# Optimization experiments

Measured on AMD Instinct MI355X. Metric: run time of the kernel, lower is better.

The kernel has to match this reference:

```python
import jax, jax.numpy as jnp
import numpy as np

B, HW, D = 16, 3600, 512
LC, NL = 768, 20
KC, VC, H = 512, 512, 8
EPS = 1e-5


def instance_norm(x):
    # x: [B, N, C]; InstanceNorm1d normalizes over the length dim N per (sample, channel),
    # biased variance, no affine (torch default).
    mu = jnp.mean(x, axis=1, keepdims=True)
    var = jnp.mean((x - mu) ** 2, axis=1, keepdims=True)
    return (x - mu) / jnp.sqrt(var + EPS)


def setup_inputs() -> dict:
    key = jax.random.key(0)
    ks = jax.random.split(key, 16)
    x = jax.random.normal(ks[0], (B, HW, D), dtype=jnp.float32)
    l = jax.random.normal(ks[1], (B, LC, NL), dtype=jnp.float32)
    # 0/1 padding mask; guarantee at least the first token is valid
    lengths = jax.random.randint(ks[2], (B, 1), 5, NL + 1)
    l_mask = (jnp.arange(NL)[None, :] < lengths).astype(jnp.float32)[:, :, None]  # [B,NL,1]
    s = 0.02
    params = dict(
        Wvis=jax.random.normal(ks[3], (D, D)) * s, bvis=jnp.zeros((D,)),
        Wq=jax.random.normal(ks[4], (KC, D)) * s, bq=jnp.zeros((KC,)),
        Wk=jax.random.normal(ks[5], (KC, LC)) * s, bk=jnp.zeros((KC,)),
        Wval=jax.random.normal(ks[6], (VC, LC)) * s, bval=jnp.zeros((VC,)),
        Ww=jax.random.normal(ks[7], (VC, VC)) * s, bw=jnp.zeros((VC,)),
        Wmm=jax.random.normal(ks[8], (VC, VC)) * s, bmm=jnp.zeros((VC,)),
    )
    return {"x": x, "l": l, "l_mask": l_mask, **params}


def reference(x, l, l_mask, Wvis, bvis, Wq, bq, Wk, bk, Wval, bval, Ww, bw, Wmm, bmm):
    b, hw, d = x.shape
    mask = l_mask[..., 0][:, None, :]  # [B,1,NL]
    # vis branch: Conv1d(dim,dim,1) + GELU (exact) + Dropout(0)
    vis = jax.nn.gelu(x @ Wvis.T + bvis, approximate=False)  # [B,HW,D]
    # query: Conv1d(v_in,KC,1) then InstanceNorm1d over HW
    q = instance_norm(x @ Wq.T + bq)  # [B,HW,KC]
    # key/value: Conv1d over language channels, then mask
    k = (jnp.einsum('kc,bcn->bkn', Wk, l) + bk[None, :, None]) * mask    # [B,KC,NL]
    v = (jnp.einsum('vc,bcn->bvn', Wval, l) + bval[None, :, None]) * mask  # [B,VC,NL]
    qh = q.reshape(b, hw, H, KC // H).transpose(0, 2, 1, 3)   # [B,H,HW,KC/H]
    kh = k.reshape(b, H, KC // H, NL)                         # [B,H,KC/H,NL]
    vh = v.reshape(b, H, VC // H, NL)                         # [B,H,VC/H,NL]
    sim = jnp.einsum('bhqd,bhdn->bhqn', qh, kh) * (KC ** -0.5)
    sim = sim + (10000.0 * mask[:, :, None, :] - 10000.0)     # additive mask bias
    attn = jax.nn.softmax(sim, axis=-1)
    out = jnp.einsum('bhqn,bhdn->bhqd', attn, vh)             # [B,H,HW,VC/H]
    out = out.transpose(0, 2, 1, 3).reshape(b, hw, VC)
    lang = instance_norm(out @ Ww.T + bw)                     # W: Conv1d + IN over HW
    mm = jax.nn.gelu((vis * lang) @ Wmm.T + bmm, approximate=False)
    return mm  # [B,HW,VC]
```

## Files before the change

### kernel.cpp

```cpp
#include <hip/hip_runtime.h>


#define B_   16
#define HW_  3600
#define D_   512
#define LC_  768
#define NL_  20

typedef __attribute__((ext_vector_type(8))) __bf16 bf16x8;
typedef __attribute__((ext_vector_type(4))) float f32x4;
typedef __attribute__((ext_vector_type(4))) float float4v;
typedef __attribute__((ext_vector_type(8))) unsigned short ushort8v;
typedef __attribute__((ext_vector_type(4))) unsigned short ushort4v;
typedef __attribute__((ext_vector_type(2))) unsigned int uint2v;

static __device__ __forceinline__ float bf2f(unsigned short u){
  unsigned int x = ((unsigned int)u) << 16; float f;
  __builtin_memcpy(&f, &x, 4); return f;
}
static __device__ __forceinline__ unsigned short f2bf(float f){
  __bf16 h = (__bf16)f;
  unsigned short u; __builtin_memcpy(&u, &h, 2); return u;
}
static __device__ __forceinline__ unsigned int pack2bf(float lo, float hi){
  return (unsigned int)f2bf(lo) | ((unsigned int)f2bf(hi) << 16);
}
static __device__ __forceinline__ float gelu_f(float x){
  float z  = x * 0.7071067811865476f;
  float az = fabsf(z);
  float t = 1.0f / fmaf(0.3275911f, az, 1.0f);
  float p = fmaf(1.061405429f, t, -1.453152027f);
  p = fmaf(p, t, 1.421413741f);
  p = fmaf(p, t, -0.284496736f);
  p = fmaf(p, t, 0.254829592f);
  p = p * t;
  float er = 1.0f - p * __expf(-az * az);
  er = copysignf(er, z);
  return 0.5f * x * (1.0f + er);
}

__global__ void k_cvt_all(const float* __restrict__ x,
                          const float* __restrict__ Wvis, const float* __restrict__ Wq,
                          const float* __restrict__ Ww,   const float* __restrict__ Wmm,
                          unsigned short* __restrict__ xb, unsigned short* __restrict__ wcat,
                          unsigned short* __restrict__ wwb, unsigned short* __restrict__ wmmb){
  const int NX4 = (B_ * HW_ * D_) / 4;
  const int TOT = NX4 + 4 * 65536;
  int i = blockIdx.x * 256 + threadIdx.x;
  int stride = gridDim.x * 256;
  for (; i < TOT; i += stride){
    const float4v* s; ushort4v* dp;
    if (i < NX4){
      s  = (const float4v*)x + i;
      dp = (ushort4v*)xb + i;
    } else {
      int k = i - NX4;
      int seg = k >> 16, o = k & 0xFFFF;
      if      (seg == 0){ s = (const float4v*)Wvis + o; dp = (ushort4v*)wcat + o; }
      else if (seg == 1){ s = (const float4v*)Wq   + o; dp = (ushort4v*)wcat + 65536 + o; }
      else if (seg == 2){ s = (const float4v*)Ww   + o; dp = (ushort4v*)wwb + o; }
      else              { s = (const float4v*)Wmm  + o; dp = (ushort4v*)wmmb + o; }
    }
    float4v v = *s;
    ushort4v u;
    u.x = f2bf(v.x); u.y = f2bf(v.y); u.z = f2bf(v.z); u.w = f2bf(v.w);
    *dp = u;
  }
}

__global__ void k_kv(const float* __restrict__ l, const float* __restrict__ l_mask,
                     const float* __restrict__ Wk, const float* __restrict__ bk,
                     const float* __restrict__ Wval, const float* __restrict__ bval,
                     float* __restrict__ k_s, float* __restrict__ v_s){
  const int b = blockIdx.y;
  const int part = blockIdx.x;
  const bool isK = part < 8;
  const int c0 = (part & 7) * 64;
  const float* W  = isK ? Wk : Wval;
  const float* bi = isK ? bk : bval;
  float* outp = isK ? k_s : v_s;

  __shared__ float l_sh[LC_ * NL_];
  for (int i = threadIdx.x; i < LC_ * NL_; i += 256)
    l_sh[i] = l[(size_t)b * LC_ * NL_ + i];
  __syncthreads();

  const int tid = threadIdx.x;
  const int cl = tid >> 2;
  const int q  = tid & 3;
  const int c  = c0 + cl;
  const float* wrow = W + (size_t)c * LC_;
  float acc[5] = {0.f,0.f,0.f,0.f,0.f};
  for (int i = 0; i < LC_; ++i){
    float wv = wrow[i];
    const float* lr = l_sh + i * NL_ + q * 5;
    acc[0] = fmaf(wv, lr[0], acc[0]);
    acc[1] = fmaf(wv, lr[1], acc[1]);
    acc[2] = fmaf(wv, lr[2], acc[2]);
    acc[3] = fmaf(wv, lr[3], acc[3]);
    acc[4] = fmaf(wv, lr[4], acc[4]);
  }
  const float bb = bi[c];
  #pragma unroll
  for (int n5 = 0; n5 < 5; ++n5){
    int n = q * 5 + n5;
    float m = l_mask[b * NL_ + n];
    float val = (acc[n5] + bb) * m;
    if (isK) val *= 0.04419417382415922f;
    outp[((size_t)b * 512 + c) * NL_ + n] = val;
  }
}

template<int MODE, int NT, bool STATS>
__global__ __launch_bounds__(256, 4) void k_gemm(
    const unsigned short* __restrict__ A,
    const unsigned short* __restrict__ Bm,
    const float* __restrict__ bias0, const float* __restrict__ bias1,
    unsigned short* __restrict__ o0, unsigned short* __restrict__ o1,
    float* __restrict__ of, float2* __restrict__ partial)
{
  __shared__ __align__(16) unsigned short smem[2][2][128 * 32];
  __shared__ float2 red[2][128];

  const int nwg = 29 * NT * B_;
  const int per = nwg >> 3;
  const int d = blockIdx.x;
  const int g = (d & 7) * per + (d >> 3);
  constexpr int NSH = (NT == 8) ? 3 : 2;
  const int nt = g & (NT - 1);
  const int rem = g >> NSH;
  const int mt = rem % 29;
  const int b  = rem / 29;

  const int m0 = mt * 128;
  const int n0 = nt * 128;
  const int tid = threadIdx.x;
  const int w = tid >> 6, lane = tid & 63;
  const int wr = w >> 1, wc = w & 1;
  const int lr_ = lane & 15, lg_ = lane >> 4;
  const int mvalid = HW_ - m0;
  const unsigned short* Ab = A + (size_t)b * HW_ * 512;

  f32x4 acc[4][4];
  #pragma unroll
  for (int i = 0; i < 4; ++i)
    #pragma unroll
    for (int j = 0; j < 4; ++j)
      acc[i][j] = (f32x4){0.f, 0.f, 0.f, 0.f};

  auto stage = [&](int kt, int buf){
    const int k0 = kt * 32;
    #pragma unroll
    for (int s = 0; s < 2; ++s){
      int chunk = s * 256 + tid;
      int row = chunk >> 2, part = chunk & 3;
      int psrc = part ^ ((row >> 1) & 3);
      int grow = row < mvalid ? row : (mvalid - 1);
      const unsigned short* gsrc = Ab + ((size_t)(m0 + grow) * 512 + k0 + psrc * 8);
      unsigned short* ldst = &smem[0][buf][(s * 256 + w * 64) * 8];
      __builtin_amdgcn_global_load_lds((const __attribute__((address_space(1))) void*)gsrc,
                                       (__attribute__((address_space(3))) void*)ldst, 16, 0, 0);
    }
    #pragma unroll
    for (int s = 0; s < 2; ++s){
      int chunk = s * 256 + tid;
      int row = chunk >> 2, part = chunk & 3;
      int psrc = part ^ ((row >> 1) & 3);
      const unsigned short* gsrc = Bm + ((size_t)(n0 + row) * 512 + k0 + psrc * 8);
      unsigned short* ldst = &smem[1][buf][(s * 256 + w * 64) * 8];
      __builtin_amdgcn_global_load_lds((const __attribute__((address_space(1))) void*)gsrc,
                                       (__attribute__((address_space(3))) void*)ldst, 16, 0, 0);
    }
  };

  auto compute = [&](int buf){
    const unsigned short* lA = &smem[0][buf][(wr * 64) * 32];
    const unsigned short* lB = &smem[1][buf][(wc * 64) * 32];
    const int kx = (lg_ ^ ((lr_ >> 1) & 3)) * 8;
    bf16x8 av[4], bv[4];
    #pragma unroll
    for (int i = 0; i < 4; ++i) av[i] = *(const bf16x8*)(lA + (i * 16 + lr_) * 32 + kx);
    #pragma unroll
    for (int j = 0; j < 4; ++j) bv[j] = *(const bf16x8*)(lB + (j * 16 + lr_) * 32 + kx);
    #pragma unroll
    for (int i = 0; i < 4; ++i)
      #pragma unroll
      for (int j = 0; j < 4; ++j)
        acc[i][j] = __builtin_amdgcn_mfma_f32_16x16x32_bf16(av[i], bv[j], acc[i][j], 0, 0, 0);
  };

  stage(0, 0);
  #pragma unroll
  for (int t = 0; t < 16; ++t){
    asm volatile("s_waitcnt lgkmcnt(0)" ::: "memory");
    __builtin_amdgcn_sched_barrier(0);
    asm volatile("s_waitcnt vmcnt(0)" ::: "memory");
    __builtin_amdgcn_s_barrier();
    __builtin_amdgcn_sched_barrier(0);
    if (t < 15) stage(t + 1, (t + 1) & 1);
    compute(t & 1);
  }

  const int colbase = n0 + wc * 64;
  float bsv[4];
  #pragma unroll
  for (int j = 0; j < 4; ++j){
    int col = colbase + j * 16 + lr_;
    if (MODE == 0) bsv[j] = (col < 512) ? bias0[col] : bias1[col - 512];
    else           bsv[j] = bias0[col];
  }
  const bool do_stats = STATS && (MODE != 0 || n0 >= 512);

  if (STATS && do_stats){
    float colsum[4] = {0.f,0.f,0.f,0.f}, colsq[4] = {0.f,0.f,0.f,0.f};
    #pragma unroll
    for (int i = 0; i < 4; ++i){
      int rowb = m0 + wr * 64 + i * 16 + lg_ * 4;
      #pragma unroll
      for (int rr = 0; rr < 4; ++rr){
        if (rowb + rr < HW_){
          #pragma unroll
          for (int j = 0; j < 4; ++j){
            float v = acc[i][j][rr] + bsv[j];
            colsum[j] += v;
            colsq[j]  = fmaf(v, v, colsq[j]);
          }
        }
      }
    }
    #pragma unroll
    for (int j = 0; j < 4; ++j){
      colsum[j] += __shfl_xor(colsum[j], 16);
      colsum[j] += __shfl_xor(colsum[j], 32);
      colsq[j]  += __shfl_xor(colsq[j], 16);
      colsq[j]  += __shfl_xor(colsq[j], 32);
    }
    if (lg_ == 0){
      #pragma unroll
      for (int j = 0; j < 4; ++j)
        red[wr][wc * 64 + j * 16 + lr_] = make_float2(colsum[j], colsq[j]);
    }
  }

  __syncthreads();

  if (STATS && do_stats && tid < 128){
    float2 r0 = red[0][tid], r1 = red[1][tid];
    int gcol = n0 + tid - (MODE == 0 ? 512 : 0);
    partial[((size_t)b * 29 + mt) * 512 + gcol] = make_float2(r0.x + r1.x, r0.y + r1.y);
  }

  unsigned short* stw = &smem[0][0][0] + w * 4096;

  if (MODE == 2){
    float* stgf = (float*)stw;
    #pragma unroll
    for (int half = 0; half < 2; ++half){
      #pragma unroll
      for (int i2 = 0; i2 < 2; ++i2){
        int i = half * 2 + i2;
        #pragma unroll
        for (int rr = 0; rr < 4; ++rr)
          #pragma unroll
          for (int j = 0; j < 4; ++j)
            stgf[(i2 * 16 + lg_ * 4 + rr) * 64 + j * 16 + lr_] = gelu_f(acc[i][j][rr] + bsv[j]);
      }
      #pragma unroll
      for (int pass = 0; pass < 8; ++pass){
        int chunk = pass * 64 + lane;
        int row = chunk >> 4, sub = chunk & 15;
        float4v vv = *(const float4v*)(stgf + row * 64 + sub * 4);
        int grow = m0 + wr * 64 + half * 32 + row;
        if (grow < HW_)
          *(float4v*)(of + ((size_t)b * HW_ + grow) * 512 + colbase + sub * 4) = vv;
      }
    }
  } else {
    #pragma unroll
    for (int i = 0; i < 4; ++i)
      #pragma unroll
      for (int rr = 0; rr < 4; ++rr)
        #pragma unroll
        for (int j = 0; j < 4; ++j){
          float v = acc[i][j][rr] + bsv[j];
          stw[(i * 16 + lg_ * 4 + rr) * 64 + j * 16 + lr_] = f2bf(v);
        }
    unsigned short* optr = (MODE == 1 || n0 < 512) ? o0 : o1;
    const int coloff = (MODE == 1 || n0 < 512) ? colbase : (colbase - 512);
    #pragma unroll
    for (int pass = 0; pass < 8; ++pass){
      int chunk = pass * 64 + lane;
      int row = chunk >> 3, sub = chunk & 7;
      ushort8v vv = *(const ushort8v*)(stw + row * 64 + sub * 8);
      int grow = m0 + wr * 64 + row;
      if (grow < HW_)
        *(ushort8v*)(optr + ((size_t)b * HW_ + grow) * 512 + coloff + sub * 8) = vv;
    }
  }
}

__global__ void k_stats_p2b(const float2* __restrict__ partial, float2* __restrict__ stats){
  const int b = blockIdx.x;
  const int c = threadIdx.x;
  float s = 0.f, q = 0.f;
  for (int mt = 0; mt < 29; ++mt){
    float2 p = partial[((size_t)b * 29 + mt) * 512 + c];
    s += p.x; q += p.y;
  }
  float mean = s * (1.0f / (float)HW_);
  float var  = q * (1.0f / (float)HW_) - mean * mean;
  stats[(size_t)b * 512 + c] = make_float2(mean, rsqrtf(var + 1e-5f));
}

__global__ void k_prep(const float2* __restrict__ partial, const float* __restrict__ k_s,
                       const float* __restrict__ v_s, const float* __restrict__ l_mask,
                       unsigned short* __restrict__ k2, unsigned short* __restrict__ v2,
                       float* __restrict__ e_s)
{
  const int b = blockIdx.x;
  const int tid = threadIdx.x;
  __shared__ float wred[4][NL_];
  __shared__ float2 stats_sh[512];

  #pragma unroll
  for (int half = 0; half < 2; ++half){
    int c = tid + half * 256;
    float s = 0.f, q = 0.f;
    for (int mt = 0; mt < 29; ++mt){
      float2 p = partial[((size_t)b * 29 + mt) * 512 + c];
      s += p.x; q += p.y;
    }
    float mean = s * (1.0f / (float)HW_);
    float var  = q * (1.0f / (float)HW_) - mean * mean;
    stats_sh[c] = make_float2(mean, rsqrtf(var + 1e-5f));
  }
  __syncthreads();

  float part[NL_];
  #pragma unroll
  for (int n = 0; n < NL_; ++n) part[n] = 0.f;
  #pragma unroll
  for (int half = 0; half < 2; ++half){
    int c = tid + half * 256;
    float2 st = stats_sh[c];
    float ms = st.x * st.y;
    const float* row = k_s + ((size_t)b * 512 + c) * NL_;
    #pragma unroll
    for (int n = 0; n < NL_; ++n) part[n] = fmaf(ms, row[n], part[n]);
  }
  #pragma unroll
  for (int n = 0; n < NL_; ++n){
    float v = part[n];
    v += __shfl_xor(v, 1);  v += __shfl_xor(v, 2);  v += __shfl_xor(v, 4);
    v += __shfl_xor(v, 8);  v += __shfl_xor(v, 16); v += __shfl_xor(v, 32);
    part[n] = v;
  }
  if ((tid & 63) == 0){
    #pragma unroll
    for (int n = 0; n < NL_; ++n) wred[tid >> 6][n] = part[n];
  }
  __syncthreads();
  if (tid < 32){
    float e;
    if (tid < NL_){
      float dsum = wred[0][tid] + wred[1][tid] + wred[2][tid] + wred[3][tid];
      e = -dsum - 10000.0f * (1.0f - l_mask[b * NL_ + tid]);
    } else {
      e = -1e30f;
    }
    e_s[b * 32 + tid] = e;
  }

  for (int i = tid; i < 16384; i += 256){
    int h = i >> 11, t = (i >> 10) & 1, s = (i >> 9) & 1;
    int l = (i >> 3) & 63, j = i & 7;
    int r = l & 15, g = l >> 4;
    int n = t * 16 + r;
    int c = h * 64 + s * 32 + g * 8 + j;
    unsigned short val = 0;
    if (n < NL_){
      float inv = stats_sh[c].y;
      val = f2bf(inv * k_s[((size_t)b * 512 + c) * NL_ + n]);
    }
    k2[(size_t)b * 16384 + i] = val;
  }
  for (int i = tid; i < 16384; i += 256){
    int h = i >> 11, ct = (i >> 9) & 3;
    int l = (i >> 3) & 63, j = i & 7;
    int r = l & 15, g = l >> 4;
    int n = g * 8 + j;
    int c = h * 64 + ct * 16 + r;
    unsigned short val = 0;
    if (n < NL_) val = f2bf(v_s[((size_t)b * 512 + c) * NL_ + n]);
    v2[(size_t)b * 16384 + i] = val;
  }
}

__global__ __launch_bounds__(256) void k_attn2(unsigned short* __restrict__ qraw,
    const unsigned short* __restrict__ k2, const unsigned short* __restrict__ v2,
    const float* __restrict__ e_s)
{
  const int b = blockIdx.y;
  const int w = threadIdx.x >> 6;
  const int tile = blockIdx.x * 4 + w;
  __shared__ __align__(16) unsigned short p_sh[4][16 * 32];
  __shared__ __align__(16) unsigned short o_sh[4][16 * 72];
  if (tile >= 225) return;
  const int lane = threadIdx.x & 63;
  const int r = lane & 15, g = lane >> 4;
  const int row0 = tile * 16;

  float4v e0 = *(const float4v*)(e_s + b * 32 + g * 4);
  float4v e1 = *(const float4v*)(e_s + b * 32 + 16 + g * 4);

  bf16x8 qf[8][2];
  const unsigned short* qbase = qraw + ((size_t)(b * HW_ + row0 + r) * 512) + g * 8;
  #pragma unroll
  for (int h = 0; h < 8; ++h)
    #pragma unroll
    for (int s = 0; s < 2; ++s)
      qf[h][s] = *(const bf16x8*)(qbase + h * 64 + s * 32);

  const unsigned short* kb = k2 + (size_t)b * 16384 + lane * 8;
  const unsigned short* vb = v2 + (size_t)b * 16384 + lane * 8;
  unsigned short* psh = &p_sh[w][0];
  unsigned short* osh = &o_sh[w][0];

  for (int h = 0; h < 8; ++h){
    bf16x8 kf00 = *(const bf16x8*)(kb + (h * 4 + 0) * 512);
    bf16x8 kf01 = *(const bf16x8*)(kb + (h * 4 + 1) * 512);
    bf16x8 kf10 = *(const bf16x8*)(kb + (h * 4 + 2) * 512);
    bf16x8 kf11 = *(const bf16x8*)(kb + (h * 4 + 3) * 512);
    f32x4 c0 = (f32x4){0.f,0.f,0.f,0.f};
    f32x4 c1 = (f32x4){0.f,0.f,0.f,0.f};
    c0 = __builtin_amdgcn_mfma_f32_16x16x32_bf16(kf00, qf[h][0], c0, 0, 0, 0);
    c0 = __builtin_amdgcn_mfma_f32_16x16x32_bf16(kf01, qf[h][1], c0, 0, 0, 0);
    c1 = __builtin_amdgcn_mfma_f32_16x16x32_bf16(kf10, qf[h][0], c1, 0, 0, 0);
    c1 = __builtin_amdgcn_mfma_f32_16x16x32_bf16(kf11, qf[h][1], c1, 0, 0, 0);

    float l0[4], l1[4];
    #pragma unroll
    for (int i = 0; i < 4; ++i){ l0[i] = c0[i] + e0[i]; l1[i] = c1[i] + e1[i]; }
    float m = fmaxf(fmaxf(fmaxf(l0[0], l0[1]), fmaxf(l0[2], l0[3])),
                    fmaxf(fmaxf(l1[0], l1[1]), fmaxf(l1[2], l1[3])));
    m = fmaxf(m, __shfl_xor(m, 16));
    m = fmaxf(m, __shfl_xor(m, 32));
    float p0[4], p1[4];
    #pragma unroll
    for (int i = 0; i < 4; ++i){ p0[i] = __expf(l0[i] - m); p1[i] = __expf(l1[i] - m); }

    uint2v pw0, pw1;
    pw0.x = pack2bf(p0[0], p0[1]); pw0.y = pack2bf(p0[2], p0[3]);
    pw1.x = pack2bf(p1[0], p1[1]); pw1.y = pack2bf(p1[2], p1[3]);
    float sum = bf2f((unsigned short)(pw0.x & 0xffff)) + bf2f((unsigned short)(pw0.x >> 16))
              + bf2f((unsigned short)(pw0.y & 0xffff)) + bf2f((unsigned short)(pw0.y >> 16))
              + bf2f((unsigned short)(pw1.x & 0xffff)) + bf2f((unsigned short)(pw1.x >> 16))
              + bf2f((unsigned short)(pw1.y & 0xffff)) + bf2f((unsigned short)(pw1.y >> 16));
    sum += __shfl_xor(sum, 16);
    sum += __shfl_xor(sum, 32);
    float inv = 1.0f / sum;

    *(uint2v*)(psh + r * 32 + 4 * g)      = pw0;
    *(uint2v*)(psh + r * 32 + 16 + 4 * g) = pw1;
    bf16x8 pfrag = *(const bf16x8*)(psh + r * 32 + g * 8);

    f32x4 dd[4];
    #pragma unroll
    for (int ct = 0; ct < 4; ++ct){
      bf16x8 vf = *(const bf16x8*)(vb + (h * 4 + ct) * 512);
      f32x4 z = (f32x4){0.f,0.f,0.f,0.f};
      dd[ct] = __builtin_amdgcn_mfma_f32_16x16x32_bf16(vf, pfrag, z, 0, 0, 0);
    }
    #pragma unroll
    for (int ct = 0; ct < 4; ++ct){
      uint2v ow;
      ow.x = pack2bf(dd[ct][0] * inv, dd[ct][1] * inv);
      ow.y = pack2bf(dd[ct][2] * inv, dd[ct][3] * inv);
      *(uint2v*)(osh + r * 72 + ct * 16 + 4 * g) = ow;
    }
    int frow = lane >> 2, fch = lane & 3;
    ushort8v t0 = *(const ushort8v*)(osh + frow * 72 + fch * 16);
    ushort8v t1 = *(const ushort8v*)(osh + frow * 72 + fch * 16 + 8);
    unsigned short* gdst = qraw + ((size_t)(b * HW_ + row0 + frow) * 512) + h * 64 + fch * 16;
    *(ushort8v*)(gdst)     = t0;
    *(ushort8v*)(gdst + 8) = t1;
  }
}

__global__ __launch_bounds__(256) void k_hmul(unsigned short* __restrict__ yw,
    const unsigned short* __restrict__ visb, const float2* __restrict__ stats)
{
  const int b = blockIdx.y, blk = blockIdx.x;
  const int w = threadIdx.x >> 6, lane = threadIdx.x & 63;
  const int c0 = lane * 8;
  float mean[8], inv[8];
  #pragma unroll
  for (int j = 0; j < 8; ++j){
    float2 st = stats[(size_t)b * 512 + c0 + j];
    mean[j] = st.x; inv[j] = st.y;
  }
  for (int it = 0; it < 30; ++it){
    int row = blk * 120 + it * 4 + w;
    size_t off = ((size_t)b * HW_ + row) * 512 + c0;
    ushort8v yv = *(const ushort8v*)(yw + off);
    ushort8v vv = *(const ushort8v*)(visb + off);
    ushort8v hv;
    #pragma unroll
    for (int j = 0; j < 8; ++j){
      float lang = (bf2f(yv[j]) - mean[j]) * inv[j];
      float visg = gelu_f(bf2f(vv[j]));
      hv[j] = f2bf(visg * lang);
    }
    *(ushort8v*)(yw + off) = hv;
  }
}

extern "C" void kernel_launch(void* const* d_in, const int* in_sizes, int n_in,
                              void* d_out, int out_size, void* d_ws, size_t ws_size,
                              hipStream_t stream)
{
  const float* x     = (const float*)d_in[0];
  const float* l     = (const float*)d_in[1];
  const float* lmask = (const float*)d_in[2];
  const float* Wvis  = (const float*)d_in[3];
  const float* bvis  = (const float*)d_in[4];
  const float* Wq    = (const float*)d_in[5];
  const float* bq    = (const float*)d_in[6];
  const float* Wk    = (const float*)d_in[7];
  const float* bk    = (const float*)d_in[8];
  const float* Wval  = (const float*)d_in[9];
  const float* bval  = (const float*)d_in[10];
  const float* Ww    = (const float*)d_in[11];
  const float* bw    = (const float*)d_in[12];
  const float* Wmm   = (const float*)d_in[13];
  const float* bmm   = (const float*)d_in[14];
  float* out = (float*)d_out;

  char* ws = (char*)d_ws;
  if (ws_size < 240517120ull) return;
  unsigned short* xb    = (unsigned short*)(ws + 0);
  unsigned short* visb  = (unsigned short*)(ws + 58982400);
  unsigned short* qraw  = (unsigned short*)(ws + 117964800);
  unsigned short* yw    = (unsigned short*)(ws + 176947200);
  unsigned short* wcat  = (unsigned short*)(ws + 235929600);
  unsigned short* wwb   = (unsigned short*)(ws + 236978176);
  unsigned short* wmmb  = (unsigned short*)(ws + 237502464);
  float*  k_s    = (float*)(ws + 238026752);
  float*  v_s    = (float*)(ws + 238682112);
  float2* stats_w= (float2*)(ws + 240451584);
  unsigned short* k2 = (unsigned short*)(ws + 0);
  unsigned short* v2 = (unsigned short*)(ws + 524288);
  float*          e_s = (float*)(ws + 1048576);
  float2* partial_q = (float2*)(ws + 176947200);
  float2* partial_w = (float2*)(ws + 1052672);

  k_cvt_all<<<2048, 256, 0, stream>>>(x, Wvis, Wq, Ww, Wmm, xb, wcat, wwb, wmmb);

  k_kv<<<dim3(16, B_), 256, 0, stream>>>(l, lmask, Wk, bk, Wval, bval, k_s, v_s);

  k_gemm<0, 8, true><<<29 * 8 * B_, 256, 0, stream>>>(xb, wcat, bvis, bq, visb, qraw, nullptr, partial_q);

  k_prep<<<B_, 256, 0, stream>>>(partial_q, k_s, v_s, lmask, k2, v2, e_s);

  k_attn2<<<dim3(57, B_), 256, 0, stream>>>(qraw, k2, v2, e_s);

  k_gemm<1, 4, true><<<29 * 4 * B_, 256, 0, stream>>>(qraw, wwb, bw, nullptr, yw, nullptr, nullptr, partial_w);

  k_stats_p2b<<<B_, 512, 0, stream>>>(partial_w, stats_w);

  k_hmul<<<dim3(30, B_), 256, 0, stream>>>(yw, visb, stats_w);

  k_gemm<2, 4, false><<<29 * 4 * B_, 256, 0, stream>>>(yw, wmmb, bmm, nullptr, nullptr, nullptr, out, nullptr);
}
```

Measured before the change: 357.6 us.

## Fuse fp32-to-bf16 conversion of x into first GEMM's A-tile staging

Drops the separate pass that converts x (about 118MB of fp32) to bf16. The first GEMM now loads fp32 A tiles into registers, converts them and writes them to LDS after compute, overlapping with the MFMA work. The per-block LDS reduction of column stats is replaced by writing per-warp-row partials directly to global memory, which doubles the partial buffer and the reads in the stats kernels. Launch bounds rise to 5 waves per SIMD. The trade-off is extra register pressure and fp32 global reads inside the GEMM, which now reads twice the bytes for the A operand.

```diff
diff --git a/kernel.cpp b/kernel.cpp
--- a/kernel.cpp
+++ b/kernel.cpp
@@ -39,28 +39,20 @@
   return 0.5f * x * (1.0f + er);
 }
 
-__global__ void k_cvt_all(const float* __restrict__ x,
-                          const float* __restrict__ Wvis, const float* __restrict__ Wq,
-                          const float* __restrict__ Ww,   const float* __restrict__ Wmm,
-                          unsigned short* __restrict__ xb, unsigned short* __restrict__ wcat,
-                          unsigned short* __restrict__ wwb, unsigned short* __restrict__ wmmb){
-  const int NX4 = (B_ * HW_ * D_) / 4;
-  const int TOT = NX4 + 4 * 65536;
+__global__ void k_cvt_w(const float* __restrict__ Wvis, const float* __restrict__ Wq,
+                        const float* __restrict__ Ww,   const float* __restrict__ Wmm,
+                        unsigned short* __restrict__ wcat,
+                        unsigned short* __restrict__ wwb, unsigned short* __restrict__ wmmb){
+  const int TOT = 4 * 65536;
   int i = blockIdx.x * 256 + threadIdx.x;
   int stride = gridDim.x * 256;
   for (; i < TOT; i += stride){
+    int seg = i >> 16, o = i & 0xFFFF;
     const float4v* s; ushort4v* dp;
-    if (i < NX4){
-      s  = (const float4v*)x + i;
-      dp = (ushort4v*)xb + i;
-    } else {
-      int k = i - NX4;
-      int seg = k >> 16, o = k & 0xFFFF;
-      if      (seg == 0){ s = (const float4v*)Wvis + o; dp = (ushort4v*)wcat + o; }
-      else if (seg == 1){ s = (const float4v*)Wq   + o; dp = (ushort4v*)wcat + 65536 + o; }
-      else if (seg == 2){ s = (const float4v*)Ww   + o; dp = (ushort4v*)wwb + o; }
-      else              { s = (const float4v*)Wmm  + o; dp = (ushort4v*)wmmb + o; }
-    }
+    if      (seg == 0){ s = (const float4v*)Wvis + o; dp = (ushort4v*)wcat + o; }
+    else if (seg == 1){ s = (const float4v*)Wq   + o; dp = (ushort4v*)wcat + 65536 + o; }
+    else if (seg == 2){ s = (const float4v*)Ww   + o; dp = (ushort4v*)wwb + o; }
+    else              { s = (const float4v*)Wmm  + o; dp = (ushort4v*)wmmb + o; }
     float4v v = *s;
     ushort4v u;
     u.x = f2bf(v.x); u.y = f2bf(v.y); u.z = f2bf(v.z); u.w = f2bf(v.w);
@@ -111,16 +103,16 @@
   }
 }
 
-template<int MODE, int NT, bool STATS>
-__global__ __launch_bounds__(256, 4) void k_gemm(
+template<int MODE, int NT, bool STATS, bool AF32>
+__global__ __launch_bounds__(256, 5) void k_gemm(
     const unsigned short* __restrict__ A,
+    const float* __restrict__ Afp,
     const unsigned short* __restrict__ Bm,
     const float* __restrict__ bias0, const float* __restrict__ bias1,
     unsigned short* __restrict__ o0, unsigned short* __restrict__ o1,
     float* __restrict__ of, float2* __restrict__ partial)
 {
   __shared__ __align__(16) unsigned short smem[2][2][128 * 32];
-  __shared__ float2 red[2][128];
 
   const int nwg = 29 * NT * B_;
   const int per = nwg >> 3;
@@ -140,6 +132,7 @@
   const int lr_ = lane & 15, lg_ = lane >> 4;
   const int mvalid = HW_ - m0;
   const unsigned short* Ab = A + (size_t)b * HW_ * 512;
+  const float* Afb = Afp + (size_t)b * HW_ * 512;
 
   f32x4 acc[4][4];
   #pragma unroll
@@ -148,7 +141,7 @@
     for (int j = 0; j < 4; ++j)
       acc[i][j] = (f32x4){0.f, 0.f, 0.f, 0.f};
 
-  auto stage = [&](int kt, int buf){
+  auto stageA = [&](int kt, int buf){
     const int k0 = kt * 32;
     #pragma unroll
     for (int s = 0; s < 2; ++s){
@@ -161,6 +154,34 @@
       __builtin_amdgcn_global_load_lds((const __attribute__((address_space(1))) void*)gsrc,
                                        (__attribute__((address_space(3))) void*)ldst, 16, 0, 0);
     }
+  };
+  float4v Ar[2][2];
+  auto issueA = [&](int kt){
+    const int k0 = kt * 32;
+    #pragma unroll
+    for (int s = 0; s < 2; ++s){
+      int chunk = s * 256 + tid;
+      int row = chunk >> 2, part = chunk & 3;
+      int psrc = part ^ ((row >> 1) & 3);
+      int grow = row < mvalid ? row : (mvalid - 1);
+      const float* gs = Afb + ((size_t)(m0 + grow) * 512 + k0 + psrc * 8);
+      Ar[s][0] = *(const float4v*)(gs);
+      Ar[s][1] = *(const float4v*)(gs + 4);
+    }
+  };
+  auto writeA = [&](int buf){
+    #pragma unroll
+    for (int s = 0; s < 2; ++s){
+      ushort8v o;
+      o[0] = f2bf(Ar[s][0].x); o[1] = f2bf(Ar[s][0].y);
+      o[2] = f2bf(Ar[s][0].z); o[3] = f2bf(Ar[s][0].w);
+      o[4] = f2bf(Ar[s][1].x); o[5] = f2bf(Ar[s][1].y);
+      o[6] = f2bf(Ar[s][1].z); o[7] = f2bf(Ar[s][1].w);
+      *(ushort8v*)(&smem[0][buf][(s * 256 + tid) * 8]) = o;
+    }
+  };
+  auto stageB = [&](int kt, int buf){
+    const int k0 = kt * 32;
     #pragma unroll
     for (int s = 0; s < 2; ++s){
       int chunk = s * 256 + tid;
@@ -189,7 +210,15 @@
         acc[i][j] = __builtin_amdgcn_mfma_f32_16x16x32_bf16(av[i], bv[j], acc[i][j], 0, 0, 0);
   };
 
-  stage(0, 0);
+  if (AF32){
+    issueA(0);
+    stageB(0, 0);
+    writeA(0);
+  } else {
+    stageA(0, 0);
+    stageB(0, 0);
+  }
+
   #pragma unroll
   for (int t = 0; t < 16; ++t){
     asm volatile("s_waitcnt lgkmcnt(0)" ::: "memory");
@@ -197,8 +226,15 @@
     asm volatile("s_waitcnt vmcnt(0)" ::: "memory");
     __builtin_amdgcn_s_barrier();
     __builtin_amdgcn_sched_barrier(0);
-    if (t < 15) stage(t + 1, (t + 1) & 1);
+    const int nb = (t + 1) & 1;
+    if (t < 15){
+      if (AF32) issueA(t + 1);
+      else      stageA(t + 1, nb);
+      stageB(t + 1, nb);
+      if (AF32) __builtin_amdgcn_sched_barrier(0);
+    }
     compute(t & 1);
+    if (AF32 && t < 15) writeA(nb);
   }
 
   const int colbase = n0 + wc * 64;
@@ -237,18 +273,15 @@
     }
     if (lg_ == 0){
       #pragma unroll
-      for (int j = 0; j < 4; ++j)
-        red[wr][wc * 64 + j * 16 + lr_] = make_float2(colsum[j], colsq[j]);
+      for (int j = 0; j < 4; ++j){
+        int gcol = colbase + j * 16 + lr_ - (MODE == 0 ? 512 : 0);
+        partial[((size_t)b * 29 + mt) * 1024 + wr * 512 + gcol] =
+          make_float2(colsum[j], colsq[j]);
+      }
     }
   }
 
   __syncthreads();
-
-  if (STATS && do_stats && tid < 128){
-    float2 r0 = red[0][tid], r1 = red[1][tid];
-    int gcol = n0 + tid - (MODE == 0 ? 512 : 0);
-    partial[((size_t)b * 29 + mt) * 512 + gcol] = make_float2(r0.x + r1.x, r0.y + r1.y);
-  }
 
   unsigned short* stw = &smem[0][0][0] + w * 4096;
 
@@ -304,8 +337,9 @@
   const int c = threadIdx.x;
   float s = 0.f, q = 0.f;
   for (int mt = 0; mt < 29; ++mt){
-    float2 p = partial[((size_t)b * 29 + mt) * 512 + c];
-    s += p.x; q += p.y;
+    float2 p0 = partial[((size_t)b * 29 + mt) * 1024 + c];
+    float2 p1 = partial[((size_t)b * 29 + mt) * 1024 + 512 + c];
+    s += p0.x + p1.x; q += p0.y + p1.y;
   }
   float mean = s * (1.0f / (float)HW_);
   float var  = q * (1.0f / (float)HW_) - mean * mean;
@@ -327,8 +361,9 @@
     int c = tid + half * 256;
     float s = 0.f, q = 0.f;
     for (int mt = 0; mt < 29; ++mt){
-      float2 p = partial[((size_t)b * 29 + mt) * 512 + c];
-      s += p.x; q += p.y;
+      float2 p0 = partial[((size_t)b * 29 + mt) * 1024 + c];
+      float2 p1 = partial[((size_t)b * 29 + mt) * 1024 + 512 + c];
+      s += p0.x + p1.x; q += p0.y + p1.y;
     }
     float mean = s * (1.0f / (float)HW_);
     float var  = q * (1.0f / (float)HW_) - mean * mean;
@@ -538,7 +573,6 @@
 
   char* ws = (char*)d_ws;
   if (ws_size < 240517120ull) return;
-  unsigned short* xb    = (unsigned short*)(ws + 0);
   unsigned short* visb  = (unsigned short*)(ws + 58982400);
   unsigned short* qraw  = (unsigned short*)(ws + 117964800);
   unsigned short* yw    = (unsigned short*)(ws + 176947200);
@@ -554,21 +588,21 @@
   float2* partial_q = (float2*)(ws + 176947200);
   float2* partial_w = (float2*)(ws + 1052672);
 
-  k_cvt_all<<<2048, 256, 0, stream>>>(x, Wvis, Wq, Ww, Wmm, xb, wcat, wwb, wmmb);
+  k_cvt_w<<<512, 256, 0, stream>>>(Wvis, Wq, Ww, Wmm, wcat, wwb, wmmb);
 
   k_kv<<<dim3(16, B_), 256, 0, stream>>>(l, lmask, Wk, bk, Wval, bval, k_s, v_s);
 
-  k_gemm<0, 8, true><<<29 * 8 * B_, 256, 0, stream>>>(xb, wcat, bvis, bq, visb, qraw, nullptr, partial_q);
+  k_gemm<0, 8, true, true><<<29 * 8 * B_, 256, 0, stream>>>(nullptr, x, wcat, bvis, bq, visb, qraw, nullptr, partial_q);
 
   k_prep<<<B_, 256, 0, stream>>>(partial_q, k_s, v_s, lmask, k2, v2, e_s);
 
   k_attn2<<<dim3(57, B_), 256, 0, stream>>>(qraw, k2, v2, e_s);
 
-  k_gemm<1, 4, true><<<29 * 4 * B_, 256, 0, stream>>>(qraw, wwb, bw, nullptr, yw, nullptr, nullptr, partial_w);
+  k_gemm<1, 4, true, false><<<29 * 4 * B_, 256, 0, stream>>>(qraw, x, wwb, bw, nullptr, yw, nullptr, nullptr, partial_w);
 
   k_stats_p2b<<<B_, 512, 0, stream>>>(partial_w, stats_w);
 
   k_hmul<<<dim3(30, B_), 256, 0, stream>>>(yw, visb, stats_w);
 
-  k_gemm<2, 4, false><<<29 * 4 * B_, 256, 0, stream>>>(yw, wmmb, bmm, nullptr, nullptr, nullptr, out, nullptr);
-}
+  k_gemm<2, 4, false, false><<<29 * 4 * B_, 256, 0, stream>>>(yw, x, wmmb, bmm, nullptr, nullptr, nullptr, out, nullptr);
+}
```

Result: slower. 823.1 us (+130.1%).
